# Optimization experiments

Measured on AMD Instinct MI355X. Metric: run time of the kernel, lower is better.

Reference implementation:

```python
import jax, jax.numpy as jnp
import numpy as np

N_NODES = 128   # num_nodes
BATCH = 4096
HIDDEN = 32     # fixed by the module's Linear(N+1, 32)


def setup_inputs() -> dict:
    key = jax.random.key(0)
    ks = jax.random.split(key, 8)
    N, B, H = N_NODES, BATCH, HIDDEN
    x = jax.random.normal(ks[0], (B, N), dtype=jnp.float32)
    # adjacency masks: A[b, :, j] = parent indicator of node j in sample b
    A = (jax.random.uniform(ks[1], (B, N, N)) < 0.3).astype(jnp.float32)
    # per-sample topological permutation
    order = jax.vmap(lambda k: jax.random.permutation(k, N))(
        jax.random.split(ks[2], B)).astype(jnp.int32)
    # intervention target per sample, -1 = no intervention
    do_idxs = jax.random.randint(ks[3], (B,), -1, N, dtype=jnp.int32)
    # externalized intervention noise (torch.normal in the original forward)
    u = jax.random.normal(ks[4], (B,), dtype=jnp.float32)
    # stacked per-node MLP params: Linear(N+1, 32) -> LeakyReLU -> Linear(32, 1)
    W1 = jax.random.normal(ks[5], (N, N + 1, H), dtype=jnp.float32) / np.sqrt(N + 1)
    b1 = jnp.zeros((N, H), dtype=jnp.float32)
    W2 = jax.random.normal(ks[6], (N, H, 1), dtype=jnp.float32) / np.sqrt(H)
    b2 = jnp.zeros((N, 1), dtype=jnp.float32)
    return dict(x=x, A=A, u=u, W1=W1, b1=b1, W2=W2, b2=b2,
                order=order, do_idxs=do_idxs)


def reference(x, A, u, W1, b1, W2, b2, order, do_idxs):
    B, N = x.shape
    bidx = jnp.arange(B)
    # set intervened entries: outputs[b, do_idxs[b]] = u[b] where do_idxs != -1
    outputs0 = jnp.where(do_idxs[:, None] == jnp.arange(N)[None, :],
                         u[:, None], jnp.zeros_like(x))

    def step(outputs, node):           # node: [B] current node per sample
        mask = A[bidx, :, node]        # [B, N] parent mask of this node
        ins = jnp.concatenate([mask * outputs,
                               x[bidx, node][:, None]], axis=1)  # [B, N+1]
        # per-node MLP gathered by node id (grouped tiny GEMMs)
        h = jax.nn.leaky_relu(jnp.einsum('bd,bdh->bh', ins, W1[node]) + b1[node])
        out = (jnp.einsum('bh,bho->bo', h, W2[node]) + b2[node])[:, 0]  # [B]
        # intervened samples keep their value u (they are skipped in the original)
        new_val = jnp.where(do_idxs == node, outputs[bidx, node], out)
        return outputs.at[bidx, node].set(new_val), None

    outputs, _ = jax.lax.scan(step, outputs0, order.T)  # sequential topo order
    return outputs
```

## Files before the change

kernel.cpp:

```cpp
#include <hip/hip_runtime.h>
#include <stdint.h>

#define NN 128
#define BB 4096
#define HH 32

__global__ __launch_bounds__(256) void pack_bits(const float* __restrict__ A,
                                                 ulonglong2* __restrict__ bitsT) {
    int tid = blockIdx.x * 256 + threadIdx.x;
    int b = tid >> 7;
    int node = tid & 127;
    const float* Ab = A + (size_t)b * NN * NN + node;
    unsigned long long w0 = 0, w1 = 0;
#pragma unroll 8
    for (int d = 0; d < 64; ++d) {
        float v = __builtin_nontemporal_load(&Ab[d * NN]);
        if (v != 0.f) w0 |= 1ull << d;
    }
#pragma unroll 8
    for (int d = 0; d < 64; ++d) {
        float v = __builtin_nontemporal_load(&Ab[(d + 64) * NN]);
        if (v != 0.f) w1 |= 1ull << d;
    }
    ulonglong2 r; r.x = w0; r.y = w1;
    bitsT[tid] = r;
}

__global__ __launch_bounds__(64) void cond_mlp(
    const float* __restrict__ x, const float* __restrict__ u,
    const float* __restrict__ W1, const float* __restrict__ b1,
    const float* __restrict__ W2, const float* __restrict__ b2,
    const int* __restrict__ order, const int* __restrict__ do_idxs,
    const ulonglong2* __restrict__ bitsT, float* __restrict__ out)
{
    const int b = blockIdx.x;
    const int lane = threadIdx.x;
    const int j = lane & 31;
    const int half = lane >> 5;

    __shared__ float2 ent[132];

    const float ub = u[b];
    const int dob = do_idxs[b];
    float out0 = (dob == lane) ? ub : 0.f;
    float out1 = (dob == lane + 64) ? ub : 0.f;

    const int* ord = order + b * NN;
    const ulonglong2* bb = bitsT + (size_t)b * NN;

    int node = ord[0];
    ulonglong2 bits = bb[node];

    for (int t = 0; t < NN; ++t) {
        const int node_n = (t < NN - 1) ? ord[t + 1] : 0;
        const ulonglong2 bits_n = bb[node_n];

        const float* Wn = W1 + (size_t)node * (NN + 1) * HH;
        const float w2v = W2[node * HH + j];
        const float b1v = b1[node * HH + j];
        const float xv  = x[b * NN + node];
        const float b2v = b2[node];

        unsigned long long bal0 = __ballot(out0 != 0.f) & bits.x;
        unsigned long long bal1 = __ballot(out1 != 0.f) & bits.y;
        const int c0 = __popcll(bal0);
        const int cnt = c0 + __popcll(bal1);
        const unsigned long long below = (1ull << lane) - 1;
        if (bal0 & (1ull << lane)) {
            int p = __popcll(bal0 & below);
            ent[p] = make_float2(out0, __int_as_float(lane));
        }
        if (bal1 & (1ull << lane)) {
            int p = c0 + __popcll(bal1 & below);
            ent[p] = make_float2(out1, __int_as_float(lane + 64));
        }
        const int cnt4 = (cnt + 3) & ~3;
        if (lane < cnt4 - cnt) ent[cnt + lane] = make_float2(0.f, __int_as_float(0));
        __syncthreads();

        float acc0 = 0.f, acc1 = 0.f;
        for (int k = 0; k < cnt4; k += 4) {
            float2 eA = ent[k + half];
            float2 eB = ent[k + 2 + half];
            int dA = __float_as_int(eA.y);
            int dB = __float_as_int(eB.y);
            acc0 += eA.x * Wn[dA * HH + j];
            acc1 += eB.x * Wn[dB * HH + j];
        }
        __syncthreads();

        float acc = acc0 + acc1;
        acc += __shfl_xor(acc, 32);
        acc += xv * Wn[NN * HH + j];
        acc += b1v;
        const float hv = (acc > 0.f) ? acc : 0.01f * acc;

        float p = hv * w2v;
        p += __shfl_xor(p, 16);
        p += __shfl_xor(p, 8);
        p += __shfl_xor(p, 4);
        p += __shfl_xor(p, 2);
        p += __shfl_xor(p, 1);
        const float outv = p + b2v;

        if (dob != node) {
            if (lane == (node & 63)) {
                if (node < 64) out0 = outv; else out1 = outv;
            }
        }
        node = node_n;
        bits = bits_n;
    }

    out[b * NN + lane] = out0;
    out[b * NN + 64 + lane] = out1;
}

extern "C" void kernel_launch(void* const* d_in, const int* in_sizes, int n_in,
                              void* d_out, int out_size, void* d_ws, size_t ws_size,
                              hipStream_t stream) {
    const float* x   = (const float*)d_in[0];
    const float* A   = (const float*)d_in[1];
    const float* u   = (const float*)d_in[2];
    const float* W1  = (const float*)d_in[3];
    const float* b1  = (const float*)d_in[4];
    const float* W2  = (const float*)d_in[5];
    const float* b2  = (const float*)d_in[6];
    const int* order = (const int*)d_in[7];
    const int* dox   = (const int*)d_in[8];

    ulonglong2* bitsT = (ulonglong2*)d_ws;

    pack_bits<<<(BB * NN) / 256, 256, 0, stream>>>(A, bitsT);
    cond_mlp<<<BB, 64, 0, stream>>>(x, u, W1, b1, W2, b2, order, dox,
                                    bitsT, (float*)d_out);
}
```

Baseline: 540.5 us.

## Vectorize adjacency bit packing and split MLP gather across two wavefronts

The bit-packing kernel now loads four adjacency columns per thread with float4 reads and builds four masks at once, instead of scalar strided nontemporal loads. The conditional MLP kernel runs two wavefronts per sample and splits the parent-gather loop four ways, merging partial sums through shared memory. This aims to cut memory transactions in the packing pass and shorten the per-step serial dependent-load chain. In exchange, each topological step gains an extra barrier and a shared-memory exchange.

```diff
diff --git a/kernel.cpp b/kernel.cpp
--- a/kernel.cpp
+++ b/kernel.cpp
@@ -6,27 +6,27 @@
 #define HH 32
 
 __global__ __launch_bounds__(256) void pack_bits(const float* __restrict__ A,
-                                                 ulonglong2* __restrict__ bitsT) {
-    int tid = blockIdx.x * 256 + threadIdx.x;
-    int b = tid >> 7;
-    int node = tid & 127;
-    const float* Ab = A + (size_t)b * NN * NN + node;
-    unsigned long long w0 = 0, w1 = 0;
+                                                 unsigned long long* __restrict__ bitsW) {
+    int t = blockIdx.x * 256 + threadIdx.x;
+    int n4 = t & 31;
+    int h  = (t >> 5) & 1;
+    int b  = t >> 6;
+    const float4* Ap = (const float4*)(A + (size_t)b * NN * NN + (size_t)h * 64 * NN) + n4;
+    unsigned long long m0 = 0, m1 = 0, m2 = 0, m3 = 0;
 #pragma unroll 8
     for (int d = 0; d < 64; ++d) {
-        float v = __builtin_nontemporal_load(&Ab[d * NN]);
-        if (v != 0.f) w0 |= 1ull << d;
+        float4 v = Ap[(size_t)d * (NN / 4)];
+        unsigned long long bit = 1ull << d;
+        if (v.x != 0.f) m0 |= bit;
+        if (v.y != 0.f) m1 |= bit;
+        if (v.z != 0.f) m2 |= bit;
+        if (v.w != 0.f) m3 |= bit;
     }
-#pragma unroll 8
-    for (int d = 0; d < 64; ++d) {
-        float v = __builtin_nontemporal_load(&Ab[(d + 64) * NN]);
-        if (v != 0.f) w1 |= 1ull << d;
-    }
-    ulonglong2 r; r.x = w0; r.y = w1;
-    bitsT[tid] = r;
+    unsigned long long* dst = bitsW + ((size_t)b * NN + n4 * 4) * 2 + h;
+    dst[0] = m0; dst[2] = m1; dst[4] = m2; dst[6] = m3;
 }
 
-__global__ __launch_bounds__(64) void cond_mlp(
+__global__ __launch_bounds__(128) void cond_mlp(
     const float* __restrict__ x, const float* __restrict__ u,
     const float* __restrict__ W1, const float* __restrict__ b1,
     const float* __restrict__ W2, const float* __restrict__ b2,
@@ -34,11 +34,14 @@
     const ulonglong2* __restrict__ bitsT, float* __restrict__ out)
 {
     const int b = blockIdx.x;
-    const int lane = threadIdx.x;
-    const int j = lane & 31;
-    const int half = lane >> 5;
+    const int tid = threadIdx.x;
+    const int lane = tid & 63;
+    const int wv = tid >> 6;
+    const int j = tid & 31;
+    const int quarter = (tid >> 5) & 3;
 
     __shared__ float2 ent[132];
+    __shared__ float part[2][32];
 
     const float ub = u[b];
     const int dob = do_idxs[b];
@@ -65,35 +68,34 @@
         unsigned long long bal1 = __ballot(out1 != 0.f) & bits.y;
         const int c0 = __popcll(bal0);
         const int cnt = c0 + __popcll(bal1);
-        const unsigned long long below = (1ull << lane) - 1;
-        if (bal0 & (1ull << lane)) {
-            int p = __popcll(bal0 & below);
-            ent[p] = make_float2(out0, __int_as_float(lane));
-        }
-        if (bal1 & (1ull << lane)) {
-            int p = c0 + __popcll(bal1 & below);
-            ent[p] = make_float2(out1, __int_as_float(lane + 64));
-        }
         const int cnt4 = (cnt + 3) & ~3;
-        if (lane < cnt4 - cnt) ent[cnt + lane] = make_float2(0.f, __int_as_float(0));
-        __syncthreads();
-
-        float acc0 = 0.f, acc1 = 0.f;
-        for (int k = 0; k < cnt4; k += 4) {
-            float2 eA = ent[k + half];
-            float2 eB = ent[k + 2 + half];
-            int dA = __float_as_int(eA.y);
-            int dB = __float_as_int(eB.y);
-            acc0 += eA.x * Wn[dA * HH + j];
-            acc1 += eB.x * Wn[dB * HH + j];
+        if (wv == 0) {
+            const unsigned long long below = (1ull << lane) - 1;
+            if (bal0 & (1ull << lane)) {
+                int p = __popcll(bal0 & below);
+                ent[p] = make_float2(out0, __int_as_float(lane));
+            }
+            if (bal1 & (1ull << lane)) {
+                int p = c0 + __popcll(bal1 & below);
+                ent[p] = make_float2(out1, __int_as_float(lane + 64));
+            }
+            if (lane < cnt4 - cnt) ent[cnt + lane] = make_float2(0.f, __int_as_float(0));
         }
         __syncthreads();
 
-        float acc = acc0 + acc1;
+        float acc = 0.f;
+        for (int k = quarter; k < cnt4; k += 4) {
+            float2 e = ent[k];
+            acc += e.x * Wn[__float_as_int(e.y) * HH + j];
+        }
         acc += __shfl_xor(acc, 32);
-        acc += xv * Wn[NN * HH + j];
-        acc += b1v;
-        const float hv = (acc > 0.f) ? acc : 0.01f * acc;
+        if (lane < 32) part[wv][j] = acc;
+        __syncthreads();
+
+        float acc2 = acc + part[1 - wv][j];
+        acc2 += xv * Wn[NN * HH + j];
+        acc2 += b1v;
+        const float hv = (acc2 > 0.f) ? acc2 : 0.01f * acc2;
 
         float p = hv * w2v;
         p += __shfl_xor(p, 16);
@@ -112,8 +114,10 @@
         bits = bits_n;
     }
 
-    out[b * NN + lane] = out0;
-    out[b * NN + 64 + lane] = out1;
+    if (wv == 0) {
+        out[b * NN + lane] = out0;
+        out[b * NN + 64 + lane] = out1;
+    }
 }
 
 extern "C" void kernel_launch(void* const* d_in, const int* in_sizes, int n_in,
@@ -129,9 +133,9 @@
     const int* order = (const int*)d_in[7];
     const int* dox   = (const int*)d_in[8];
 
-    ulonglong2* bitsT = (ulonglong2*)d_ws;
+    unsigned long long* bitsW = (unsigned long long*)d_ws;
 
-    pack_bits<<<(BB * NN) / 256, 256, 0, stream>>>(A, bitsT);
-    cond_mlp<<<BB, 64, 0, stream>>>(x, u, W1, b1, W2, b2, order, dox,
-                                    bitsT, (float*)d_out);
+    pack_bits<<<(BB * 64) / 256, 256, 0, stream>>>(A, bitsW);
+    cond_mlp<<<BB, 128, 0, stream>>>(x, u, W1, b1, W2, b2, order, dox,
+                                     (const ulonglong2*)bitsW, (float*)d_out);
 }
```

New measurement: 611.1 us. +13.1%, slower.
